# Kernel tuning notes

Hardware: AMD Instinct MI355X
Metric: run time of the kernel (lower is better)

Reference implementation:

```python
import jax, jax.numpy as jnp
import numpy as np

B, U, V, C = 2, 8, 512, 256
H, DK = 8, 64            # num_heads, key_query_features (per head)
R = 256                  # result_features; per-head value dim R//H = 32
CODE = 192
EPS = 1e-6               # affinity renorm epsilon
LN_EPS = 1e-5            # torch LayerNorm default
GAIN = 2.5               # post_attention_gain / post_mlp_gain buffers


def _ln(x, g, b):
    m = x.mean(-1, keepdims=True)
    v = ((x - m) ** 2).mean(-1, keepdims=True)
    return (x - m) / jnp.sqrt(v + LN_EPS) * g + b


def _modlin(x, c, W, Wc, b=None):
    # ModFC / ModLin: y = W(x * (1 + Wc c)) (+ b)
    y = (x * (1.0 + c @ Wc)) @ W
    return y if b is None else y + b


def setup_inputs() -> dict:
    key = jax.random.key(0)
    ks = jax.random.split(key, 16)
    s = 0.02
    return {
        'variables': jax.random.normal(ks[0], (B, U, V, C), jnp.float32),
        'codes': jax.random.normal(ks[1], (U, CODE), jnp.float32),
        'affinities': jax.random.uniform(ks[2], (B, U, V), jnp.float32),
        'ln1_g': jnp.ones((C,), jnp.float32),
        'ln1_b': jnp.zeros((C,), jnp.float32),
        'Wq': jax.random.normal(ks[3], (C, H * DK), jnp.float32) * s,
        'Wcq': jax.random.normal(ks[4], (CODE, C), jnp.float32) * s,
        'Wk': jax.random.normal(ks[5], (C, H * DK), jnp.float32) * s,
        'Wck': jax.random.normal(ks[6], (CODE, C), jnp.float32) * s,
        'Wv': jax.random.normal(ks[7], (C, R), jnp.float32) * s,
        'Wcv': jax.random.normal(ks[8], (CODE, C), jnp.float32) * s,
        'bv': jnp.zeros((R,), jnp.float32),
        'ln2_g': jnp.ones((R,), jnp.float32),
        'ln2_b': jnp.zeros((R,), jnp.float32),
        'W1': jax.random.normal(ks[9], (R, R), jnp.float32) * s,
        'Wc1': jax.random.normal(ks[10], (CODE, R), jnp.float32) * s,
        'b1m': jnp.zeros((R,), jnp.float32),
        'W2': jax.random.normal(ks[11], (R, R), jnp.float32) * s,
        'Wc2': jax.random.normal(ks[12], (CODE, R), jnp.float32) * s,
        'b2m': jnp.zeros((R,), jnp.float32),
    }


def reference(variables, codes, affinities, ln1_g, ln1_b, Wq, Wcq, Wk, Wck,
              Wv, Wcv, bv, ln2_g, ln2_b, W1, Wc1, b1m, W2, Wc2, b2m):
    # codes: [U, code] -> broadcast to [B, U, V, code]
    c4 = jnp.broadcast_to(codes[None, :, None, :], (B, U, V, CODE))
    xn = _ln(variables, ln1_g, ln1_b)                      # b u v c
    q = _modlin(xn, c4, Wq, Wcq).reshape(B, U, V, H, DK)   # b u v h d
    k = _modlin(xn, c4, Wk, Wck).reshape(B, U, V, H, DK)
    v = _modlin(xn, c4, Wv, Wcv, bv).reshape(B, U, V, H, R // H)
    # scores: b u r s h (attention over s); scale_attention_weights=False -> scale 1
    scores = jnp.einsum('burhd,bushd->bursh', q, k)
    dot = jax.nn.softmax(scores, axis=3)                   # softmax over s (dim=-2)
    # affinity modulation: aff_r * aff_s * weights, renormalized over s
    kmw = affinities[:, :, :, None, None] * affinities[:, :, None, :, None] * dot
    kmw = kmw / (kmw.sum(axis=3, keepdims=True) + EPS)
    att = jnp.einsum('bursh,bushc->burhc', kmw, v).reshape(B, U, V, R)
    g = affinities[..., None]
    # residual_mode='gating', variable_features==result_features
    attn_out = (1.0 - g) * variables + g * GAIN * att
    yn = _ln(attn_out, ln2_g, ln2_b)
    h1 = jax.nn.gelu(_modlin(yn, c4, W1, Wc1, b1m), approximate=False)
    h2 = jax.nn.gelu(_modlin(h1, c4, W2, Wc2, b2m), approximate=False)
    mlp_out = h2 * g
    results = (1.0 - g) * attn_out + g * GAIN * mlp_out
    return results
```

## Files before the change

### kernel.cpp

```cpp
#include <hip/hip_runtime.h>
#include <math.h>

#define B_ 2
#define U_ 8
#define V_ 512
#define C_ 256
#define H_ 8
#define R_ 256
#define EPS_ 1e-6f
#define LN_EPS_ 1e-5f
#define GAIN_ 2.5f

typedef __attribute__((ext_vector_type(8))) short bf16x8;
typedef __attribute__((ext_vector_type(4))) float f32x4;
typedef unsigned short ushort_t;

__device__ __forceinline__ ushort_t f2bf(float x) {
    union { float f; unsigned u; } v; v.f = x;
    unsigned r = v.u + 0x7fffu + ((v.u >> 16) & 1u);
    return (ushort_t)(r >> 16);
}

__device__ __forceinline__ float waveReduceSum(float v) {
    #pragma unroll
    for (int m = 1; m < 64; m <<= 1) v += __shfl_xor(v, m);
    return v;
}

__device__ __forceinline__ float gelu_exact(float x) {
    return 0.5f * x * (1.f + erff(x * 0.70710678118654752f));
}

__global__ void k_mods(const float* __restrict__ codes,
                       const float* __restrict__ Wcq, const float* __restrict__ Wck,
                       const float* __restrict__ Wcv, const float* __restrict__ Wc1,
                       const float* __restrict__ Wc2, const float* __restrict__ bv,
                       float* __restrict__ mods, float* __restrict__ biasQ) {
    int u = blockIdx.x, c = threadIdx.x;
    const float* cd = codes + u * 192;
    float aq = 0.f, ak = 0.f, av = 0.f, a1 = 0.f, a2 = 0.f;
    for (int j = 0; j < 192; ++j) {
        float cj = cd[j];
        aq = fmaf(cj, Wcq[j * C_ + c], aq);
        ak = fmaf(cj, Wck[j * C_ + c], ak);
        av = fmaf(cj, Wcv[j * C_ + c], av);
        a1 = fmaf(cj, Wc1[j * R_ + c], a1);
        a2 = fmaf(cj, Wc2[j * R_ + c], a2);
    }
    mods[(0 * U_ + u) * C_ + c] = 1.f + aq;
    mods[(1 * U_ + u) * C_ + c] = 1.f + ak;
    mods[(2 * U_ + u) * C_ + c] = 1.f + av;
    mods[(3 * U_ + u) * C_ + c] = 1.f + a1;
    mods[(4 * U_ + u) * C_ + c] = 1.f + a2;
    if (u == 0) {
        biasQ[c] = 0.f; biasQ[256 + c] = 0.f; biasQ[512 + c] = 0.f;
        biasQ[768 + c] = 0.f; biasQ[1024 + c] = bv[c];
    }
}

__global__ __launch_bounds__(256) void k_fold(
    const float* __restrict__ Wq, const float* __restrict__ Wk,
    const float* __restrict__ Wv, const float* __restrict__ W1,
    const float* __restrict__ W2, const float* __restrict__ mods,
    ushort_t* __restrict__ wqkvT, ushort_t* __restrict__ w1T,
    ushort_t* __restrict__ w2T) {
    __shared__ ushort_t T[64][65];
    int id = blockIdx.x;
    const float* W; int ldw, modIdx, colAdd, tilesPerU, base;
    ushort_t* dst; int dstCols;
    if (id < 256)      { base = 0;   W = Wq; ldw = 512; modIdx = 0; colAdd = 0;    dst = wqkvT; dstCols = 1280; tilesPerU = 32; }
    else if (id < 512) { base = 256; W = Wk; ldw = 512; modIdx = 1; colAdd = 512;  dst = wqkvT; dstCols = 1280; tilesPerU = 32; }
    else if (id < 640) { base = 512; W = Wv; ldw = 256; modIdx = 2; colAdd = 1024; dst = wqkvT; dstCols = 1280; tilesPerU = 16; }
    else if (id < 768) { base = 640; W = W1; ldw = 256; modIdx = 3; colAdd = 0;    dst = w1T;  dstCols = 256;  tilesPerU = 16; }
    else               { base = 768; W = W2; ldw = 256; modIdx = 4; colAdd = 0;    dst = w2T;  dstCols = 256;  tilesPerU = 16; }
    int local = id - base;
    int u = local / tilesPerU;
    int t = local % tilesPerU;
    int nColTiles = ldw / 64;
    int c0 = (t / nColTiles) * 64;
    int col0 = (t % nColTiles) * 64;
    const float* modRow = mods + (modIdx * U_ + u) * C_;
    int tid = threadIdx.x;
    int cl = tid >> 4;
    int cg = (tid & 15) * 4;
    #pragma unroll
    for (int it = 0; it < 4; ++it) {
        int c = cl + it * 16;
        float m = modRow[c0 + c];
        float4 wv = *(const float4*)&W[(size_t)(c0 + c) * ldw + col0 + cg];
        T[c][cg + 0] = f2bf(wv.x * m);
        T[c][cg + 1] = f2bf(wv.y * m);
        T[c][cg + 2] = f2bf(wv.z * m);
        T[c][cg + 3] = f2bf(wv.w * m);
    }
    __syncthreads();
    int j = tid >> 2;
    int ch = (tid & 3) * 16;
    ushort_t tmp[16];
    #pragma unroll
    for (int i = 0; i < 16; ++i) tmp[i] = T[ch + i][j];
    ushort_t* o = dst + ((size_t)u * dstCols + colAdd + col0 + j) * 256 + c0 + ch;
    *(bf16x8*)&o[0] = *(const bf16x8*)&tmp[0];
    *(bf16x8*)&o[8] = *(const bf16x8*)&tmp[8];
}

__global__ void k_ln1(const float* __restrict__ x, const float* __restrict__ g,
                      const float* __restrict__ b, ushort_t* __restrict__ xnb) {
    int row = blockIdx.x * 4 + (threadIdx.x >> 6);
    int lane = threadIdx.x & 63;
    const float* xr = x + (size_t)row * C_;
    float4 v = *(const float4*)&xr[lane * 4];
    float s = v.x + v.y + v.z + v.w;
    float ss = v.x * v.x + v.y * v.y + v.z * v.z + v.w * v.w;
    s = waveReduceSum(s); ss = waveReduceSum(ss);
    float mean = s * (1.f / 256.f);
    float var = ss * (1.f / 256.f) - mean * mean;
    float rstd = rsqrtf(var + LN_EPS_);
    float4 gg = *(const float4*)&g[lane * 4];
    float4 bb = *(const float4*)&b[lane * 4];
    unsigned lo = (unsigned)f2bf((v.x - mean) * rstd * gg.x + bb.x)
                | ((unsigned)f2bf((v.y - mean) * rstd * gg.y + bb.y) << 16);
    unsigned hi = (unsigned)f2bf((v.z - mean) * rstd * gg.z + bb.z)
                | ((unsigned)f2bf((v.w - mean) * rstd * gg.w + bb.w) << 16);
    uint2 pk; pk.x = lo; pk.y = hi;
    *(uint2*)&xnb[(size_t)row * C_ + lane * 4] = pk;
}

template<int MODE>
__global__ __launch_bounds__(256) void k_gemm(
    const ushort_t* __restrict__ X, const ushort_t* __restrict__ WT, int wPerU,
    const float* __restrict__ bias, ushort_t* __restrict__ outB, int ldo,
    float* __restrict__ outF, const float* __restrict__ ao,
    const float* __restrict__ aff) {
    __shared__ __align__(16) ushort_t xs[64][72];
    __shared__ __align__(16) ushort_t wt[64][72];
    int col0 = blockIdx.x * 64;
    int row0 = blockIdx.y * 64;
    int u = (row0 >> 9) & 7;
    const ushort_t* Wu = WT + ((size_t)u * wPerU + col0) * 256;
    int tid = threadIdx.x;
    int w = tid >> 6, l = tid & 63;
    int lr = l & 15, lg = l >> 4;
    f32x4 acc[4] = {};
    for (int k0 = 0; k0 < 256; k0 += 64) {
        int r1 = tid >> 3, ko1 = (tid & 7) * 8;
        int r2 = (tid + 256) >> 3, ko2 = ((tid + 256) & 7) * 8;
        *(bf16x8*)&xs[r1][ko1] = *(const bf16x8*)&X[(size_t)(row0 + r1) * 256 + k0 + ko1];
        *(bf16x8*)&xs[r2][ko2] = *(const bf16x8*)&X[(size_t)(row0 + r2) * 256 + k0 + ko2];
        *(bf16x8*)&wt[r1][ko1] = *(const bf16x8*)&Wu[(size_t)r1 * 256 + k0 + ko1];
        *(bf16x8*)&wt[r2][ko2] = *(const bf16x8*)&Wu[(size_t)r2 * 256 + k0 + ko2];
        __syncthreads();
        #pragma unroll
        for (int n = 0; n < 4; ++n) {
            #pragma unroll
            for (int kk = 0; kk < 2; ++kk) {
                bf16x8 a = *(const bf16x8*)&xs[w * 16 + lr][kk * 32 + lg * 8];
                bf16x8 bb = *(const bf16x8*)&wt[n * 16 + lr][kk * 32 + lg * 8];
                acc[n] = __builtin_amdgcn_mfma_f32_16x16x32_bf16(a, bb, acc[n], 0, 0, 0);
            }
        }
        __syncthreads();
    }
    #pragma unroll
    for (int n = 0; n < 4; ++n) {
        int col = col0 + n * 16 + lr;
        float bval = bias[col];
        #pragma unroll
        for (int i = 0; i < 4; ++i) {
            int row = row0 + w * 16 + lg * 4 + i;
            float v = acc[n][i] + bval;
            if (MODE >= 1) v = gelu_exact(v);
            if (MODE == 2) {
                float a = aff[row];
                float aov = ao[(size_t)row * 256 + col];
                outF[(size_t)row * 256 + col] = (1.f - a) * aov + GAIN_ * a * a * v;
            } else {
                outB[(size_t)row * ldo + col] = f2bf(v);
            }
        }
    }
}

__global__ __launch_bounds__(256) void k_attn(
    const ushort_t* __restrict__ qkv, const float* __restrict__ aff,
    float* __restrict__ att) {
    __shared__ __align__(16) ushort_t Qs[64][72];
    __shared__ __align__(16) ushort_t Ks[64][72];
    __shared__ __align__(16) ushort_t Ps[64][72];
    __shared__ __align__(16) ushort_t Vt[32][72];
    __shared__ float As[64];
    int r0 = blockIdx.x * 64;
    int buh = blockIdx.y;
    int h = buh & 7, bu = buh >> 3;
    const ushort_t* base = qkv + (size_t)bu * 512 * 1280;
    int tid = threadIdx.x;
    int w = tid >> 6, l = tid & 63;
    int lr = l & 15, lg = l >> 4;
    {
        int rA = tid >> 3, koA = (tid & 7) * 8;
        int rB = (tid + 256) >> 3, koB = ((tid + 256) & 7) * 8;
        *(bf16x8*)&Qs[rA][koA] = *(const bf16x8*)&base[(size_t)(r0 + rA) * 1280 + h * 64 + koA];
        *(bf16x8*)&Qs[rB][koB] = *(const bf16x8*)&base[(size_t)(r0 + rB) * 1280 + h * 64 + koB];
    }
    f32x4 pacc[2] = {};
    float wsum[4] = {}, asum[4] = {};
    for (int s0 = 0; s0 < 512; s0 += 64) {
        {
            int rA = tid >> 3, koA = (tid & 7) * 8;
            int rB = (tid + 256) >> 3, koB = ((tid + 256) & 7) * 8;
            *(bf16x8*)&Ks[rA][koA] = *(const bf16x8*)&base[(size_t)(s0 + rA) * 1280 + 512 + h * 64 + koA];
            *(bf16x8*)&Ks[rB][koB] = *(const bf16x8*)&base[(size_t)(s0 + rB) * 1280 + 512 + h * 64 + koB];
        }
        {
            int c = tid & 31, sblk = (tid >> 5) * 8;
            ushort_t tmp[8];
            #pragma unroll
            for (int jj = 0; jj < 8; ++jj)
                tmp[jj] = base[(size_t)(s0 + sblk + jj) * 1280 + 1024 + h * 32 + c];
            *(bf16x8*)&Vt[c][sblk] = *(const bf16x8*)&tmp[0];
        }
        if (tid < 64) As[tid] = aff[bu * 512 + s0 + tid];
        __syncthreads();
        #pragma unroll
        for (int n = 0; n < 4; ++n) {
            f32x4 sc = {};
            #pragma unroll
            for (int kk = 0; kk < 2; ++kk) {
                bf16x8 a = *(const bf16x8*)&Qs[w * 16 + lr][kk * 32 + lg * 8];
                bf16x8 bb = *(const bf16x8*)&Ks[n * 16 + lr][kk * 32 + lg * 8];
                sc = __builtin_amdgcn_mfma_f32_16x16x32_bf16(a, bb, sc, 0, 0, 0);
            }
            int scol = n * 16 + lr;
            float av = As[scol];
            #pragma unroll
            for (int i = 0; i < 4; ++i) {
                float e = __expf(sc[i]);
                float ae = e * av;
                wsum[i] += e; asum[i] += ae;
                Ps[w * 16 + lg * 4 + i][scol] = f2bf(ae);
            }
        }
        #pragma unroll
        for (int n = 0; n < 2; ++n) {
            #pragma unroll
            for (int kk = 0; kk < 2; ++kk) {
                bf16x8 a = *(const bf16x8*)&Ps[w * 16 + lr][kk * 32 + lg * 8];
                bf16x8 bb = *(const bf16x8*)&Vt[n * 16 + lr][kk * 32 + lg * 8];
                pacc[n] = __builtin_amdgcn_mfma_f32_16x16x32_bf16(a, bb, pacc[n], 0, 0, 0);
            }
        }
        __syncthreads();
    }
    #pragma unroll
    for (int m = 1; m < 16; m <<= 1) {
        #pragma unroll
        for (int i = 0; i < 4; ++i) {
            wsum[i] += __shfl_xor(wsum[i], m);
            asum[i] += __shfl_xor(asum[i], m);
        }
    }
    #pragma unroll
    for (int i = 0; i < 4; ++i) {
        int r = r0 + w * 16 + lg * 4 + i;
        float ar = aff[bu * 512 + r];
        float scale = ar / (ar * asum[i] + EPS_ * wsum[i]);
        float* ob = att + ((size_t)bu * 512 + r) * 256 + h * 32;
        ob[lr]      = pacc[0][i] * scale;
        ob[16 + lr] = pacc[1][i] * scale;
    }
}

__global__ void k_gate_ln2(const float* __restrict__ x, const float* __restrict__ att,
                           const float* __restrict__ aff, const float* __restrict__ g2,
                           const float* __restrict__ b2, float* __restrict__ ao,
                           ushort_t* __restrict__ ynb) {
    int row = blockIdx.x * 4 + (threadIdx.x >> 6);
    int lane = threadIdx.x & 63;
    float a = aff[row];
    const float* xr = x + (size_t)row * C_;
    const float* atr = att + (size_t)row * C_;
    float4 xv = *(const float4*)&xr[lane * 4];
    float4 av = *(const float4*)&atr[lane * 4];
    float4 o;
    o.x = (1.f - a) * xv.x + a * GAIN_ * av.x;
    o.y = (1.f - a) * xv.y + a * GAIN_ * av.y;
    o.z = (1.f - a) * xv.z + a * GAIN_ * av.z;
    o.w = (1.f - a) * xv.w + a * GAIN_ * av.w;
    float s = o.x + o.y + o.z + o.w;
    float ss = o.x * o.x + o.y * o.y + o.z * o.z + o.w * o.w;
    s = waveReduceSum(s); ss = waveReduceSum(ss);
    float mean = s * (1.f / 256.f);
    float var = ss * (1.f / 256.f) - mean * mean;
    float rstd = rsqrtf(var + LN_EPS_);
    *(float4*)&ao[(size_t)row * C_ + lane * 4] = o;
    float4 gg = *(const float4*)&g2[lane * 4];
    float4 bb = *(const float4*)&b2[lane * 4];
    unsigned lo = (unsigned)f2bf((o.x - mean) * rstd * gg.x + bb.x)
                | ((unsigned)f2bf((o.y - mean) * rstd * gg.y + bb.y) << 16);
    unsigned hi = (unsigned)f2bf((o.z - mean) * rstd * gg.z + bb.z)
                | ((unsigned)f2bf((o.w - mean) * rstd * gg.w + bb.w) << 16);
    uint2 pk; pk.x = lo; pk.y = hi;
    *(uint2*)&ynb[(size_t)row * C_ + lane * 4] = pk;
}

extern "C" void kernel_launch(void* const* d_in, const int* in_sizes, int n_in,
                              void* d_out, int out_size, void* d_ws, size_t ws_size,
                              hipStream_t stream) {
    const float* variables  = (const float*)d_in[0];
    const float* codes      = (const float*)d_in[1];
    const float* affinities = (const float*)d_in[2];
    const float* ln1_g = (const float*)d_in[3];
    const float* ln1_b = (const float*)d_in[4];
    const float* Wq  = (const float*)d_in[5];
    const float* Wcq = (const float*)d_in[6];
    const float* Wk  = (const float*)d_in[7];
    const float* Wck = (const float*)d_in[8];
    const float* Wv  = (const float*)d_in[9];
    const float* Wcv = (const float*)d_in[10];
    const float* bv  = (const float*)d_in[11];
    const float* ln2_g = (const float*)d_in[12];
    const float* ln2_b = (const float*)d_in[13];
    const float* W1  = (const float*)d_in[14];
    const float* Wc1 = (const float*)d_in[15];
    const float* b1m = (const float*)d_in[16];
    const float* W2  = (const float*)d_in[17];
    const float* Wc2 = (const float*)d_in[18];
    const float* b2m = (const float*)d_in[19];

    char* p = (char*)d_ws;
    float* modsF = (float*)p;   p += 40960;
    float* biasQ = (float*)p;   p += 5120;
    float* attF  = (float*)p;   p += 8388608;
    float* aoF   = (float*)p;   p += 8388608;
    ushort_t* xnb   = (ushort_t*)p; p += 4194304;
    ushort_t* wqkvT = (ushort_t*)p; p += 5242880;
    ushort_t* w1T   = (ushort_t*)p; p += 1048576;
    ushort_t* w2T   = (ushort_t*)p; p += 1048576;
    ushort_t* qkvb  = (ushort_t*)p; p += 20971520;
    ushort_t* ynb   = (ushort_t*)p; p += 4194304;
    ushort_t* h1b   = (ushort_t*)p; p += 4194304;
    float* outp = (float*)d_out;

    k_mods<<<U_, 256, 0, stream>>>(codes, Wcq, Wck, Wcv, Wc1, Wc2, bv, modsF, biasQ);
    k_fold<<<896, 256, 0, stream>>>(Wq, Wk, Wv, W1, W2, modsF, wqkvT, w1T, w2T);
    k_ln1<<<2048, 256, 0, stream>>>(variables, ln1_g, ln1_b, xnb);
    k_gemm<0><<<dim3(20, 128), 256, 0, stream>>>(xnb, wqkvT, 1280, biasQ, qkvb, 1280,
                                                 nullptr, nullptr, nullptr);
    k_attn<<<dim3(8, 128), 256, 0, stream>>>(qkvb, affinities, attF);
    k_gate_ln2<<<2048, 256, 0, stream>>>(variables, attF, affinities, ln2_g, ln2_b, aoF, ynb);
    k_gemm<1><<<dim3(4, 128), 256, 0, stream>>>(ynb, w1T, 256, b1m, h1b, 256,
                                                nullptr, nullptr, nullptr);
    k_gemm<2><<<dim3(4, 128), 256, 0, stream>>>(h1b, w2T, 256, b2m, nullptr, 256,
                                                outp, aoF, affinities);
}
```

Baseline: 183.1 us.

## Retile QKV GEMM, emit transposed V, and prefetch K/V in attention

Splits the code-modulation kernel across 40 blocks, one per (weight, unit) pair, so it has more parallelism. Replaces the 64x64 QKV GEMM with a 128x128 tiled kernel that also writes a transposed copy of V, which removes the strided gather of V inside attention. The attention kernel now prefetches the next K/V/affinity tile into registers while computing the current one, simplifies the row-sum reductions, and remaps blocks so that a (b,u) slice stays on one XCD. In exchange it uses more registers per thread and an extra V write in the QKV epilogue.

```diff
diff --git a/kernel.cpp b/kernel.cpp
--- a/kernel.cpp
+++ b/kernel.cpp
@@ -36,23 +36,16 @@
                        const float* __restrict__ Wcv, const float* __restrict__ Wc1,
                        const float* __restrict__ Wc2, const float* __restrict__ bv,
                        float* __restrict__ mods, float* __restrict__ biasQ) {
-    int u = blockIdx.x, c = threadIdx.x;
+    int id = blockIdx.x;
+    int kind = id >> 3, u = id & 7;
+    const float* Wc = (kind == 0) ? Wcq : (kind == 1) ? Wck :
+                      (kind == 2) ? Wcv : (kind == 3) ? Wc1 : Wc2;
+    int c = threadIdx.x;
     const float* cd = codes + u * 192;
-    float aq = 0.f, ak = 0.f, av = 0.f, a1 = 0.f, a2 = 0.f;
-    for (int j = 0; j < 192; ++j) {
-        float cj = cd[j];
-        aq = fmaf(cj, Wcq[j * C_ + c], aq);
-        ak = fmaf(cj, Wck[j * C_ + c], ak);
-        av = fmaf(cj, Wcv[j * C_ + c], av);
-        a1 = fmaf(cj, Wc1[j * R_ + c], a1);
-        a2 = fmaf(cj, Wc2[j * R_ + c], a2);
-    }
-    mods[(0 * U_ + u) * C_ + c] = 1.f + aq;
-    mods[(1 * U_ + u) * C_ + c] = 1.f + ak;
-    mods[(2 * U_ + u) * C_ + c] = 1.f + av;
-    mods[(3 * U_ + u) * C_ + c] = 1.f + a1;
-    mods[(4 * U_ + u) * C_ + c] = 1.f + a2;
-    if (u == 0) {
+    float a = 0.f;
+    for (int j = 0; j < 192; ++j) a = fmaf(cd[j], Wc[j * 256 + c], a);
+    mods[id * 256 + c] = 1.f + a;
+    if (id == 0) {
         biasQ[c] = 0.f; biasQ[256 + c] = 0.f; biasQ[512 + c] = 0.f;
         biasQ[768 + c] = 0.f; biasQ[1024 + c] = bv[c];
     }
@@ -126,147 +119,160 @@
     *(uint2*)&xnb[(size_t)row * C_ + lane * 4] = pk;
 }
 
-template<int MODE>
-__global__ __launch_bounds__(256) void k_gemm(
-    const ushort_t* __restrict__ X, const ushort_t* __restrict__ WT, int wPerU,
-    const float* __restrict__ bias, ushort_t* __restrict__ outB, int ldo,
-    float* __restrict__ outF, const float* __restrict__ ao,
-    const float* __restrict__ aff) {
-    __shared__ __align__(16) ushort_t xs[64][72];
-    __shared__ __align__(16) ushort_t wt[64][72];
-    int col0 = blockIdx.x * 64;
-    int row0 = blockIdx.y * 64;
+__global__ __launch_bounds__(256) void k_qkv(
+    const ushort_t* __restrict__ X, const ushort_t* __restrict__ WT,
+    const float* __restrict__ biasQ, ushort_t* __restrict__ out,
+    ushort_t* __restrict__ vT) {
+    __shared__ __align__(16) ushort_t xs[128][72];
+    __shared__ __align__(16) ushort_t wt[128][72];
+    int col0 = blockIdx.x * 128;
+    int row0 = blockIdx.y * 128;
     int u = (row0 >> 9) & 7;
-    const ushort_t* Wu = WT + ((size_t)u * wPerU + col0) * 256;
+    const ushort_t* Wu = WT + (size_t)(u * 1280 + col0) * 256;
     int tid = threadIdx.x;
     int w = tid >> 6, l = tid & 63;
     int lr = l & 15, lg = l >> 4;
-    f32x4 acc[4] = {};
+    int wm = w >> 1, wn = w & 1;
+    f32x4 acc[4][4] = {};
+    int sr = tid >> 3, sko = (tid & 7) * 8;
     for (int k0 = 0; k0 < 256; k0 += 64) {
-        int r1 = tid >> 3, ko1 = (tid & 7) * 8;
-        int r2 = (tid + 256) >> 3, ko2 = ((tid + 256) & 7) * 8;
-        *(bf16x8*)&xs[r1][ko1] = *(const bf16x8*)&X[(size_t)(row0 + r1) * 256 + k0 + ko1];
-        *(bf16x8*)&xs[r2][ko2] = *(const bf16x8*)&X[(size_t)(row0 + r2) * 256 + k0 + ko2];
-        *(bf16x8*)&wt[r1][ko1] = *(const bf16x8*)&Wu[(size_t)r1 * 256 + k0 + ko1];
-        *(bf16x8*)&wt[r2][ko2] = *(const bf16x8*)&Wu[(size_t)r2 * 256 + k0 + ko2];
+        #pragma unroll
+        for (int it = 0; it < 4; ++it) {
+            int r = sr + it * 32;
+            *(bf16x8*)&xs[r][sko] = *(const bf16x8*)&X[(size_t)(row0 + r) * 256 + k0 + sko];
+            *(bf16x8*)&wt[r][sko] = *(const bf16x8*)&Wu[(size_t)r * 256 + k0 + sko];
+        }
         __syncthreads();
         #pragma unroll
-        for (int n = 0; n < 4; ++n) {
+        for (int m = 0; m < 4; ++m) {
             #pragma unroll
             for (int kk = 0; kk < 2; ++kk) {
-                bf16x8 a = *(const bf16x8*)&xs[w * 16 + lr][kk * 32 + lg * 8];
-                bf16x8 bb = *(const bf16x8*)&wt[n * 16 + lr][kk * 32 + lg * 8];
-                acc[n] = __builtin_amdgcn_mfma_f32_16x16x32_bf16(a, bb, acc[n], 0, 0, 0);
+                bf16x8 a = *(const bf16x8*)&xs[wm * 64 + m * 16 + lr][kk * 32 + lg * 8];
+                #pragma unroll
+                for (int n = 0; n < 4; ++n) {
+                    bf16x8 bb = *(const bf16x8*)&wt[wn * 64 + n * 16 + lr][kk * 32 + lg * 8];
+                    acc[m][n] = __builtin_amdgcn_mfma_f32_16x16x32_bf16(a, bb, acc[m][n], 0, 0, 0);
+                }
             }
         }
         __syncthreads();
     }
     #pragma unroll
-    for (int n = 0; n < 4; ++n) {
-        int col = col0 + n * 16 + lr;
-        float bval = bias[col];
-        #pragma unroll
-        for (int i = 0; i < 4; ++i) {
-            int row = row0 + w * 16 + lg * 4 + i;
-            float v = acc[n][i] + bval;
-            if (MODE >= 1) v = gelu_exact(v);
-            if (MODE == 2) {
-                float a = aff[row];
-                float aov = ao[(size_t)row * 256 + col];
-                outF[(size_t)row * 256 + col] = (1.f - a) * aov + GAIN_ * a * a * v;
-            } else {
-                outB[(size_t)row * ldo + col] = f2bf(v);
+    for (int m = 0; m < 4; ++m) {
+        int rowb = row0 + wm * 64 + m * 16 + lg * 4;
+        #pragma unroll
+        for (int n = 0; n < 4; ++n) {
+            int col = col0 + wn * 64 + n * 16 + lr;
+            float bval = biasQ[col];
+            ushort_t pk4[4];
+            #pragma unroll
+            for (int i = 0; i < 4; ++i) {
+                float v = acc[m][n][i] + bval;
+                pk4[i] = f2bf(v);
+                out[(size_t)(rowb + i) * 1280 + col] = pk4[i];
+            }
+            if (col >= 1024) {
+                int hh = (col - 1024) >> 5, cc = (col - 1024) & 31;
+                int bu = rowb >> 9;
+                uint2 pw;
+                pw.x = (unsigned)pk4[0] | ((unsigned)pk4[1] << 16);
+                pw.y = (unsigned)pk4[2] | ((unsigned)pk4[3] << 16);
+                *(uint2*)&vT[(size_t)((bu * 8 + hh) * 32 + cc) * 512 + (rowb & 511)] = pw;
             }
         }
     }
 }
 
 __global__ __launch_bounds__(256) void k_attn(
-    const ushort_t* __restrict__ qkv, const float* __restrict__ aff,
-    float* __restrict__ att) {
+    const ushort_t* __restrict__ qkv, const ushort_t* __restrict__ vT,
+    const float* __restrict__ aff, float* __restrict__ att) {
     __shared__ __align__(16) ushort_t Qs[64][72];
     __shared__ __align__(16) ushort_t Ks[64][72];
-    __shared__ __align__(16) ushort_t Ps[64][72];
+    __shared__ __align__(16) ushort_t Pt[64][72];
     __shared__ __align__(16) ushort_t Vt[32][72];
     __shared__ float As[64];
-    int r0 = blockIdx.x * 64;
-    int buh = blockIdx.y;
-    int h = buh & 7, bu = buh >> 3;
+    int id = blockIdx.x;
+    int xcd = id & 7, sl = id >> 3;
+    int bu = xcd + 8 * (sl >> 6);
+    int inr = sl & 63;
+    int h = inr & 7;
+    int r0 = (inr >> 3) * 64;
     const ushort_t* base = qkv + (size_t)bu * 512 * 1280;
+    const ushort_t* vbase = vT + (size_t)((bu * 8 + h) * 32) * 512;
     int tid = threadIdx.x;
     int w = tid >> 6, l = tid & 63;
     int lr = l & 15, lg = l >> 4;
-    {
-        int rA = tid >> 3, koA = (tid & 7) * 8;
-        int rB = (tid + 256) >> 3, koB = ((tid + 256) & 7) * 8;
-        *(bf16x8*)&Qs[rA][koA] = *(const bf16x8*)&base[(size_t)(r0 + rA) * 1280 + h * 64 + koA];
-        *(bf16x8*)&Qs[rB][koB] = *(const bf16x8*)&base[(size_t)(r0 + rB) * 1280 + h * 64 + koB];
-    }
+    int sr = tid >> 3, sko = (tid & 7) * 8;
+    *(bf16x8*)&Qs[sr][sko]      = *(const bf16x8*)&base[(size_t)(r0 + sr) * 1280 + h * 64 + sko];
+    *(bf16x8*)&Qs[sr + 32][sko] = *(const bf16x8*)&base[(size_t)(r0 + sr + 32) * 1280 + h * 64 + sko];
+    bf16x8 kr0 = *(const bf16x8*)&base[(size_t)sr * 1280 + 512 + h * 64 + sko];
+    bf16x8 kr1 = *(const bf16x8*)&base[(size_t)(sr + 32) * 1280 + 512 + h * 64 + sko];
+    bf16x8 vr  = *(const bf16x8*)&vbase[(size_t)sr * 512 + sko];
+    float afv = (tid < 64) ? aff[bu * 512 + tid] : 0.f;
+    *(bf16x8*)&Ks[sr][sko] = kr0;
+    *(bf16x8*)&Ks[sr + 32][sko] = kr1;
+    if (sr < 32) *(bf16x8*)&Vt[sr][sko] = vr;
+    if (tid < 64) As[tid] = afv;
+    __syncthreads();
+    float wsum = 0.f, asum = 0.f;
     f32x4 pacc[2] = {};
-    float wsum[4] = {}, asum[4] = {};
-    for (int s0 = 0; s0 < 512; s0 += 64) {
-        {
-            int rA = tid >> 3, koA = (tid & 7) * 8;
-            int rB = (tid + 256) >> 3, koB = ((tid + 256) & 7) * 8;
-            *(bf16x8*)&Ks[rA][koA] = *(const bf16x8*)&base[(size_t)(s0 + rA) * 1280 + 512 + h * 64 + koA];
-            *(bf16x8*)&Ks[rB][koB] = *(const bf16x8*)&base[(size_t)(s0 + rB) * 1280 + 512 + h * 64 + koB];
-        }
-        {
-            int c = tid & 31, sblk = (tid >> 5) * 8;
-            ushort_t tmp[8];
-            #pragma unroll
-            for (int jj = 0; jj < 8; ++jj)
-                tmp[jj] = base[(size_t)(s0 + sblk + jj) * 1280 + 1024 + h * 32 + c];
-            *(bf16x8*)&Vt[c][sblk] = *(const bf16x8*)&tmp[0];
-        }
-        if (tid < 64) As[tid] = aff[bu * 512 + s0 + tid];
-        __syncthreads();
+    for (int t = 0; t < 8; ++t) {
+        int s0n = (t + 1) * 64;
+        if (t < 7) {
+            kr0 = *(const bf16x8*)&base[(size_t)(s0n + sr) * 1280 + 512 + h * 64 + sko];
+            kr1 = *(const bf16x8*)&base[(size_t)(s0n + sr + 32) * 1280 + 512 + h * 64 + sko];
+            if (sr < 32) vr = *(const bf16x8*)&vbase[(size_t)sr * 512 + s0n + sko];
+            if (tid < 64) afv = aff[bu * 512 + s0n + tid];
+        }
         #pragma unroll
         for (int n = 0; n < 4; ++n) {
             f32x4 sc = {};
             #pragma unroll
             for (int kk = 0; kk < 2; ++kk) {
-                bf16x8 a = *(const bf16x8*)&Qs[w * 16 + lr][kk * 32 + lg * 8];
-                bf16x8 bb = *(const bf16x8*)&Ks[n * 16 + lr][kk * 32 + lg * 8];
-                sc = __builtin_amdgcn_mfma_f32_16x16x32_bf16(a, bb, sc, 0, 0, 0);
-            }
-            int scol = n * 16 + lr;
-            float av = As[scol];
-            #pragma unroll
-            for (int i = 0; i < 4; ++i) {
-                float e = __expf(sc[i]);
-                float ae = e * av;
-                wsum[i] += e; asum[i] += ae;
-                Ps[w * 16 + lg * 4 + i][scol] = f2bf(ae);
-            }
+                bf16x8 ka = *(const bf16x8*)&Ks[n * 16 + lr][kk * 32 + lg * 8];
+                bf16x8 qb = *(const bf16x8*)&Qs[w * 16 + lr][kk * 32 + lg * 8];
+                sc = __builtin_amdgcn_mfma_f32_16x16x32_bf16(ka, qb, sc, 0, 0, 0);
+            }
+            float4 a4 = *(const float4*)&As[n * 16 + lg * 4];
+            float e0 = __expf(sc[0]), e1 = __expf(sc[1]);
+            float e2 = __expf(sc[2]), e3 = __expf(sc[3]);
+            wsum += (e0 + e1) + (e2 + e3);
+            float ae0 = e0 * a4.x, ae1 = e1 * a4.y, ae2 = e2 * a4.z, ae3 = e3 * a4.w;
+            asum += (ae0 + ae1) + (ae2 + ae3);
+            uint2 pw;
+            pw.x = (unsigned)f2bf(ae0) | ((unsigned)f2bf(ae1) << 16);
+            pw.y = (unsigned)f2bf(ae2) | ((unsigned)f2bf(ae3) << 16);
+            *(uint2*)&Pt[w * 16 + lr][n * 16 + lg * 4] = pw;
         }
         #pragma unroll
         for (int n = 0; n < 2; ++n) {
             #pragma unroll
             for (int kk = 0; kk < 2; ++kk) {
-                bf16x8 a = *(const bf16x8*)&Ps[w * 16 + lr][kk * 32 + lg * 8];
-                bf16x8 bb = *(const bf16x8*)&Vt[n * 16 + lr][kk * 32 + lg * 8];
-                pacc[n] = __builtin_amdgcn_mfma_f32_16x16x32_bf16(a, bb, pacc[n], 0, 0, 0);
+                bf16x8 pa = *(const bf16x8*)&Pt[w * 16 + lr][kk * 32 + lg * 8];
+                bf16x8 vb = *(const bf16x8*)&Vt[n * 16 + lr][kk * 32 + lg * 8];
+                pacc[n] = __builtin_amdgcn_mfma_f32_16x16x32_bf16(pa, vb, pacc[n], 0, 0, 0);
             }
         }
         __syncthreads();
-    }
-    #pragma unroll
-    for (int m = 1; m < 16; m <<= 1) {
-        #pragma unroll
-        for (int i = 0; i < 4; ++i) {
-            wsum[i] += __shfl_xor(wsum[i], m);
-            asum[i] += __shfl_xor(asum[i], m);
-        }
-    }
+        if (t < 7) {
+            *(bf16x8*)&Ks[sr][sko] = kr0;
+            *(bf16x8*)&Ks[sr + 32][sko] = kr1;
+            if (sr < 32) *(bf16x8*)&Vt[sr][sko] = vr;
+            if (tid < 64) As[tid] = afv;
+            __syncthreads();
+        }
+    }
+    asum += __shfl_xor(asum, 16); asum += __shfl_xor(asum, 32);
+    wsum += __shfl_xor(wsum, 16); wsum += __shfl_xor(wsum, 32);
+    float ar = aff[bu * 512 + r0 + w * 16 + lr];
+    float scale = ar / (ar * asum + EPS_ * wsum);
     #pragma unroll
     for (int i = 0; i < 4; ++i) {
-        int r = r0 + w * 16 + lg * 4 + i;
-        float ar = aff[bu * 512 + r];
-        float scale = ar / (ar * asum[i] + EPS_ * wsum[i]);
-        float* ob = att + ((size_t)bu * 512 + r) * 256 + h * 32;
-        ob[lr]      = pacc[0][i] * scale;
-        ob[16 + lr] = pacc[1][i] * scale;
+        float sc_i = __shfl(scale, lg * 4 + i);
+        int q = r0 + w * 16 + lg * 4 + i;
+        float* ob = att + ((size_t)bu * 512 + q) * 256 + h * 32;
+        ob[lr]      = pacc[0][i] * sc_i;
+        ob[16 + lr] = pacc[1][i] * sc_i;
     }
 }
 
@@ -303,6 +309,60 @@
     *(uint2*)&ynb[(size_t)row * C_ + lane * 4] = pk;
 }
 
+template<int MODE>
+__global__ __launch_bounds__(256) void k_gemm(
+    const ushort_t* __restrict__ X, const ushort_t* __restrict__ WT, int wPerU,
+    const float* __restrict__ bias, ushort_t* __restrict__ outB, int ldo,
+    float* __restrict__ outF, const float* __restrict__ ao,
+    const float* __restrict__ aff) {
+    __shared__ __align__(16) ushort_t xs[64][72];
+    __shared__ __align__(16) ushort_t wt[64][72];
+    int col0 = blockIdx.x * 64;
+    int row0 = blockIdx.y * 64;
+    int u = (row0 >> 9) & 7;
+    const ushort_t* Wu = WT + ((size_t)u * wPerU + col0) * 256;
+    int tid = threadIdx.x;
+    int w = tid >> 6, l = tid & 63;
+    int lr = l & 15, lg = l >> 4;
+    f32x4 acc[4] = {};
+    for (int k0 = 0; k0 < 256; k0 += 64) {
+        int r1 = tid >> 3, ko1 = (tid & 7) * 8;
+        int r2 = (tid + 256) >> 3, ko2 = ((tid + 256) & 7) * 8;
+        *(bf16x8*)&xs[r1][ko1] = *(const bf16x8*)&X[(size_t)(row0 + r1) * 256 + k0 + ko1];
+        *(bf16x8*)&xs[r2][ko2] = *(const bf16x8*)&X[(size_t)(row0 + r2) * 256 + k0 + ko2];
+        *(bf16x8*)&wt[r1][ko1] = *(const bf16x8*)&Wu[(size_t)r1 * 256 + k0 + ko1];
+        *(bf16x8*)&wt[r2][ko2] = *(const bf16x8*)&Wu[(size_t)r2 * 256 + k0 + ko2];
+        __syncthreads();
+        #pragma unroll
+        for (int n = 0; n < 4; ++n) {
+            #pragma unroll
+            for (int kk = 0; kk < 2; ++kk) {
+                bf16x8 a = *(const bf16x8*)&xs[w * 16 + lr][kk * 32 + lg * 8];
+                bf16x8 bb = *(const bf16x8*)&wt[n * 16 + lr][kk * 32 + lg * 8];
+                acc[n] = __builtin_amdgcn_mfma_f32_16x16x32_bf16(a, bb, acc[n], 0, 0, 0);
+            }
+        }
+        __syncthreads();
+    }
+    #pragma unroll
+    for (int n = 0; n < 4; ++n) {
+        int col = col0 + n * 16 + lr;
+        float bval = bias[col];
+        #pragma unroll
+        for (int i = 0; i < 4; ++i) {
+            int row = row0 + w * 16 + lg * 4 + i;
+            float v = gelu_exact(acc[n][i] + bval);
+            if (MODE == 2) {
+                float a = aff[row];
+                float aov = ao[(size_t)row * 256 + col];
+                outF[(size_t)row * 256 + col] = (1.f - a) * aov + GAIN_ * a * a * v;
+            } else {
+                outB[(size_t)row * ldo + col] = f2bf(v);
+            }
+        }
+    }
+}
+
 extern "C" void kernel_launch(void* const* d_in, const int* in_sizes, int n_in,
                               void* d_out, int out_size, void* d_ws, size_t ws_size,
                               hipStream_t stream) {
@@ -339,14 +399,14 @@
     ushort_t* qkvb  = (ushort_t*)p; p += 20971520;
     ushort_t* ynb   = (ushort_t*)p; p += 4194304;
     ushort_t* h1b   = (ushort_t*)p; p += 4194304;
+    ushort_t* vTb   = (ushort_t*)p; p += 4194304;
     float* outp = (float*)d_out;
 
-    k_mods<<<U_, 256, 0, stream>>>(codes, Wcq, Wck, Wcv, Wc1, Wc2, bv, modsF, biasQ);
+    k_mods<<<40, 256, 0, stream>>>(codes, Wcq, Wck, Wcv, Wc1, Wc2, bv, modsF, biasQ);
     k_fold<<<896, 256, 0, stream>>>(Wq, Wk, Wv, W1, W2, modsF, wqkvT, w1T, w2T);
     k_ln1<<<2048, 256, 0, stream>>>(variables, ln1_g, ln1_b, xnb);
-    k_gemm<0><<<dim3(20, 128), 256, 0, stream>>>(xnb, wqkvT, 1280, biasQ, qkvb, 1280,
-                                                 nullptr, nullptr, nullptr);
-    k_attn<<<dim3(8, 128), 256, 0, stream>>>(qkvb, affinities, attF);
+    k_qkv<<<dim3(10, 64), 256, 0, stream>>>(xnb, wqkvT, biasQ, qkvb, vTb);
+    k_attn<<<1024, 256, 0, stream>>>(qkvb, vTb, affinities, attF);
     k_gate_ln2<<<2048, 256, 0, stream>>>(variables, attF, affinities, ln2_g, ln2_b, aoF, ynb);
     k_gemm<1><<<dim3(4, 128), 256, 0, stream>>>(ynb, w1T, 256, b1m, h1b, 256,
                                                 nullptr, nullptr, nullptr);
```

New measurement: 175.6 us. -4.1%, faster.
